# Optimization experiments

Measured on AMD Instinct MI355X. Metric: run time of the kernel, lower is better.

Reference implementation:

```python
import jax, jax.numpy as jnp
import numpy as np

N_KERNELS = 21
N_LAYERS = 2
N_HEADS = 8
ATT_DIM = 32
FF_HID = 100
EMB = 300


def kernel_mus(n):
    mus = [1.0]
    bin_size = 2.0 / (n - 1)
    mus.append(1.0 - bin_size / 2.0)
    for _ in range(1, n - 1):
        mus.append(mus[-1] - bin_size)
    return np.array(mus, dtype=np.float32)


def kernel_sigmas(n):
    return np.array([0.001] + [0.1] * (n - 1), dtype=np.float32)


def setup_inputs() -> dict:
    key = jax.random.key(0)
    ks = jax.random.split(key, 12)
    B, LQ, LD = 32, 64, 512
    u = lambda k, s, a: jax.random.uniform(k, s, jnp.float32, -a, a)
    return dict(
        q_embed=jax.random.normal(ks[0], (B, LQ, EMB), jnp.float32),
        d_embed=jax.random.normal(ks[1], (B, LD, EMB), jnp.float32),
        mask_q=(jax.random.uniform(ks[2], (B, LQ)) > 0.1).astype(jnp.float32),
        mask_d=(jax.random.uniform(ks[3], (B, LD)) > 0.1).astype(jnp.float32),
        mixer=jnp.full((1, 1, 1), 0.5, jnp.float32),
        nn_scaler=jnp.full((1,), 0.01, jnp.float32),
        ff_w1=u(ks[4], (N_LAYERS, EMB, FF_HID), 0.05),
        ff_b1=jnp.zeros((N_LAYERS, FF_HID), jnp.float32),
        ff_w2=u(ks[5], (N_LAYERS, FF_HID, EMB), 0.05),
        ff_b2=jnp.zeros((N_LAYERS, EMB), jnp.float32),
        ln1_g=jnp.ones((N_LAYERS, EMB), jnp.float32),
        ln1_b=jnp.zeros((N_LAYERS, EMB), jnp.float32),
        att_w=u(ks[6], (N_LAYERS, EMB, 3 * ATT_DIM), 0.05),
        att_b=jnp.zeros((N_LAYERS, 3 * ATT_DIM), jnp.float32),
        out_w=u(ks[7], (N_LAYERS, ATT_DIM, EMB), 0.05),
        out_b=jnp.zeros((N_LAYERS, EMB), jnp.float32),
        ln2_g=jnp.ones((N_LAYERS, EMB), jnp.float32),
        ln2_b=jnp.zeros((N_LAYERS, EMB), jnp.float32),
        dense_w=u(ks[8], (1, N_KERNELS), 0.014),
    )


def _layer_norm(x, g, b, eps=1e-6):
    m = jnp.mean(x, -1, keepdims=True)
    s = jnp.std(x, -1, keepdims=True, ddof=1)  # torch std is unbiased
    return g * (x - m) / (s + eps) + b


def _encoder(x, mask, p):
    # AllenNLP StackedSelfAttentionEncoder: [FF -> res+LN -> MHSA -> res+LN] x2
    B, T, E = x.shape
    scale = jnp.sqrt(jnp.float32(E // N_HEADS))
    hd = ATT_DIM // N_HEADS
    for l in range(N_LAYERS):
        h = jax.nn.relu(x @ p['ff_w1'][l] + p['ff_b1'][l]) @ p['ff_w2'][l] + p['ff_b2'][l]
        h = _layer_norm(h + x, p['ln1_g'][l], p['ln1_b'][l])
        c = h @ p['att_w'][l] + p['att_b'][l]              # [B,T,3*ATT_DIM]
        q = c[..., :ATT_DIM].reshape(B, T, N_HEADS, hd)
        k = c[..., ATT_DIM:2 * ATT_DIM].reshape(B, T, N_HEADS, hd)
        v = c[..., 2 * ATT_DIM:].reshape(B, T, N_HEADS, hd)
        sims = jnp.einsum('bqhd,bkhd->bhqk', q / scale, k)
        m = mask[:, None, None, :]
        att = jax.nn.softmax(sims * m, axis=-1) * m         # AllenNLP masked_softmax
        att = att / (jnp.sum(att, -1, keepdims=True) + 1e-13)
        o = jnp.einsum('bhqk,bkhd->bqhd', att, v).reshape(B, T, ATT_DIM)
        o = o @ p['out_w'][l] + p['out_b'][l]
        x = _layer_norm(o + h, p['ln2_g'][l], p['ln2_b'][l])
    return x


def reference(q_embed, d_embed, mask_q, mask_d, mixer, nn_scaler,
              ff_w1, ff_b1, ff_w2, ff_b2, ln1_g, ln1_b,
              att_w, att_b, out_w, out_b, ln2_g, ln2_b, dense_w):
    p = dict(ff_w1=ff_w1, ff_b1=ff_b1, ff_w2=ff_w2, ff_b2=ff_b2,
             ln1_g=ln1_g, ln1_b=ln1_b, att_w=att_w, att_b=att_b,
             out_w=out_w, out_b=out_b, ln2_g=ln2_g, ln2_b=ln2_b)
    mu = jnp.asarray(kernel_mus(N_KERNELS))        # [K]
    sigma = jnp.asarray(kernel_sigmas(N_KERNELS))  # [K]
    mq = mask_q[..., None]
    md = mask_d[..., None]
    q = q_embed * mq
    d = d_embed * md
    qc = _encoder(q, mask_q, p)
    dc = _encoder(d, mask_d, p)
    q = (mixer * q + (1.0 - mixer) * qc) * mq
    d = (mixer * d + (1.0 - mixer) * dc) * md
    qd_mask = mask_q[:, :, None] * mask_d[:, None, :]  # [B,Q,D]
    qn = q / (jnp.linalg.norm(q, axis=-1, keepdims=True) + 1e-13)
    dn = d / (jnp.linalg.norm(d, axis=-1, keepdims=True) + 1e-13)
    cos = jnp.einsum('bqe,bde->bqd', qn, dn) * qd_mask
    # Gaussian RBF soft histogram: [B,Q,D,K]
    kr = jnp.exp(-(cos[..., None] - mu) ** 2 / (2.0 * sigma ** 2)) * qd_mask[..., None]
    pkq = jnp.sum(kr, axis=2)                                 # [B,Q,K]
    log_pkq = jnp.log2(jnp.clip(pkq, 1e-10)) * nn_scaler
    per_kernel = jnp.sum(log_pkq * mq, axis=1)                # [B,K]
    return jnp.squeeze(per_kernel @ dense_w.T, axis=1)        # [B]
```

## Files before the change

### kernel.cpp

```cpp
#include <hip/hip_runtime.h>
#include <hip/hip_bf16.h>

#define BATCH 32
#define LQ 64
#define LD 512
#define EMB 300
#define FFH 100
#define ATTD 32
#define NH 8
#define NK 21
#define MQ (BATCH * LQ)
#define MD (BATCH * LD)
#define MALL (MQ + MD)

typedef __attribute__((ext_vector_type(8))) short bf16x8;
typedef __attribute__((ext_vector_type(4))) float f32x4;

__device__ __forceinline__ float wave_sum(float v) {
    #pragma unroll
    for (int off = 32; off > 0; off >>= 1) v += __shfl_xor(v, off);
    return v;
}

__device__ __forceinline__ float bf2f(__hip_bfloat16 h) {
    return __bfloat162float(h);
}

__device__ __forceinline__ float4 bf4_to_f4(const __hip_bfloat16* p) {
    uint2 u = *(const uint2*)p;
    float4 f;
    f.x = __uint_as_float((u.x & 0xffffu) << 16);
    f.y = __uint_as_float(u.x & 0xffff0000u);
    f.z = __uint_as_float((u.y & 0xffffu) << 16);
    f.w = __uint_as_float(u.y & 0xffff0000u);
    return f;
}

__global__ void maskmul_all(const float* __restrict__ q_embed, const float* __restrict__ d_embed,
                            const float* __restrict__ mask_q, const float* __restrict__ mask_d,
                            __hip_bfloat16* __restrict__ xbf, float* __restrict__ mall) {
    int i = blockIdx.x * blockDim.x + threadIdx.x;
    if (i >= MALL * EMB) return;
    int tok = i / EMB;
    float m, v;
    if (tok < MQ) {
        m = mask_q[tok];
        v = q_embed[i];
    } else {
        m = mask_d[tok - MQ];
        v = d_embed[i - MQ * EMB];
    }
    xbf[i] = __float2bfloat16(v * m);
    if (i % EMB == 0) mall[tok] = m;
}

__device__ __forceinline__ void conv_seg(const float* __restrict__ w, __hip_bfloat16* __restrict__ wt,
                                         int j, int K, int N) {
    int l = j / (K * N);
    int r = j % (K * N);
    int k = r / N, n = r % N;
    wt[(size_t)l * N * K + (size_t)n * K + k] = __float2bfloat16(w[j]);
}
__global__ void convert_all(const float* __restrict__ w1, const float* __restrict__ w2,
                            const float* __restrict__ aw, const float* __restrict__ ow,
                            __hip_bfloat16* __restrict__ w1t, __hip_bfloat16* __restrict__ w2t,
                            __hip_bfloat16* __restrict__ awt, __hip_bfloat16* __restrict__ owt) {
    int i = blockIdx.x * blockDim.x + threadIdx.x;
    const int S1 = 2 * EMB * FFH;
    const int S2 = S1 + 2 * FFH * EMB;
    const int S3 = S2 + 2 * EMB * 96;
    const int S4 = S3 + 2 * ATTD * EMB;
    if (i < S1)       conv_seg(w1, w1t, i, EMB, FFH);
    else if (i < S2)  conv_seg(w2, w2t, i - S1, FFH, EMB);
    else if (i < S3)  conv_seg(aw, awt, i - S2, EMB, 96);
    else if (i < S4)  conv_seg(ow, owt, i - S3, ATTD, EMB);
}

__device__ __forceinline__ void stage_row8(const __hip_bfloat16* __restrict__ src, bool rowvalid,
                                           int K, int gk, __hip_bfloat16* dst) {
    if (rowvalid && gk + 8 <= K) {
        const uint2* p = (const uint2*)(src + gk);
        uint2 a = p[0], b = p[1];
        *(uint2*)dst = a;
        *(uint2*)(dst + 4) = b;
    } else {
        #pragma unroll
        for (int j = 0; j < 8; j++)
            dst[j] = (rowvalid && gk + j < K) ? src[gk + j] : __float2bfloat16(0.f);
    }
}

template <bool RELU>
__global__ __launch_bounds__(256) void gemm_mfma(const __hip_bfloat16* __restrict__ A,
                                                 const __hip_bfloat16* __restrict__ Bt,
                                                 const float* __restrict__ bias,
                                                 __hip_bfloat16* __restrict__ Cb,
                                                 int M, int N, int K) {
    __shared__ __align__(16) __hip_bfloat16 As[64][40];
    __shared__ __align__(16) __hip_bfloat16 Bs[64][40];
    const int tid = threadIdx.x;
    const int m0 = blockIdx.y * 64, n0 = blockIdx.x * 64;
    const int lane = tid & 63;
    const int wv = tid >> 6;
    const int wm = wv >> 1, wn = wv & 1;
    const int l15 = lane & 15, lg = lane >> 4;
    const int srow = tid >> 2, sk8 = (tid & 3) * 8;
    f32x4 acc[2][2] = {};
    const int NS = (K + 31) >> 5;
    const __hip_bfloat16* arow = A + (size_t)(m0 + srow) * K;
    const bool bvalid = (n0 + srow) < N;
    const __hip_bfloat16* brow = Bt + (size_t)(n0 + srow) * K;

    for (int s = 0; s < NS; s++) {
        const int gk = (s << 5) + sk8;
        if (s) __syncthreads();
        stage_row8(arow, true, K, gk, &As[srow][sk8]);
        stage_row8(brow, bvalid, K, gk, &Bs[srow][sk8]);
        __syncthreads();
        bf16x8 af0 = *(const bf16x8*)&As[wm * 32 + l15][lg * 8];
        bf16x8 af1 = *(const bf16x8*)&As[wm * 32 + 16 + l15][lg * 8];
        bf16x8 bf0 = *(const bf16x8*)&Bs[wn * 32 + l15][lg * 8];
        bf16x8 bf1 = *(const bf16x8*)&Bs[wn * 32 + 16 + l15][lg * 8];
        acc[0][0] = __builtin_amdgcn_mfma_f32_16x16x32_bf16(af0, bf0, acc[0][0], 0, 0, 0);
        acc[0][1] = __builtin_amdgcn_mfma_f32_16x16x32_bf16(af0, bf1, acc[0][1], 0, 0, 0);
        acc[1][0] = __builtin_amdgcn_mfma_f32_16x16x32_bf16(af1, bf0, acc[1][0], 0, 0, 0);
        acc[1][1] = __builtin_amdgcn_mfma_f32_16x16x32_bf16(af1, bf1, acc[1][1], 0, 0, 0);
    }

    #pragma unroll
    for (int fc = 0; fc < 2; fc++) {
        int col = n0 + wn * 32 + fc * 16 + l15;
        if (col >= N) continue;
        float bs = bias[col];
        #pragma unroll
        for (int fr = 0; fr < 2; fr++) {
            int rbase = m0 + wm * 32 + fr * 16 + lg * 4;
            #pragma unroll
            for (int r = 0; r < 4; r++) {
                int row = rbase + r;
                float v = acc[fr][fc][r] + bs;
                if (RELU) v = fmaxf(v, 0.f);
                Cb[(size_t)row * N + col] = __float2bfloat16(v);
            }
        }
    }
}

__global__ __launch_bounds__(256) void gemm_ln(const __hip_bfloat16* __restrict__ A,
                                               const __hip_bfloat16* __restrict__ Bt,
                                               const float* __restrict__ bias,
                                               const __hip_bfloat16* __restrict__ Res,
                                               const float* __restrict__ g,
                                               const float* __restrict__ beta,
                                               __hip_bfloat16* __restrict__ Y,
                                               int M, int K) {
    __shared__ __align__(16) __hip_bfloat16 As[32][40];
    __shared__ __align__(16) __hip_bfloat16 Bs[320][40];
    __shared__ float red[2][4][32];
    const int tid = threadIdx.x;
    const int m0 = blockIdx.x * 32;
    const int lane = tid & 63;
    const int wv = tid >> 6;
    const int l15 = lane & 15, lg = lane >> 4;
    const int c0 = wv * 80;
    f32x4 acc[2][5] = {};
    const int NS = (K + 31) >> 5;

    for (int s = 0; s < NS; s++) {
        const int gk0 = s << 5;
        if (s) __syncthreads();
        for (int ch = tid; ch < 1408; ch += 256) {
            if (ch < 128) {
                int row = ch >> 2, k8 = (ch & 3) * 8;
                stage_row8(A + (size_t)(m0 + row) * K, true, K, gk0 + k8, &As[row][k8]);
            } else {
                int cc = ch - 128;
                int row = cc >> 2, k8 = (cc & 3) * 8;
                stage_row8(Bt + (size_t)row * K, row < EMB, K, gk0 + k8, &Bs[row][k8]);
            }
        }
        __syncthreads();
        bf16x8 af[2], bfr[5];
        af[0] = *(const bf16x8*)&As[l15][lg * 8];
        af[1] = *(const bf16x8*)&As[16 + l15][lg * 8];
        #pragma unroll
        for (int fc = 0; fc < 5; fc++)
            bfr[fc] = *(const bf16x8*)&Bs[c0 + fc * 16 + l15][lg * 8];
        #pragma unroll
        for (int fr = 0; fr < 2; fr++)
            #pragma unroll
            for (int fc = 0; fc < 5; fc++)
                acc[fr][fc] = __builtin_amdgcn_mfma_f32_16x16x32_bf16(af[fr], bfr[fc], acc[fr][fc], 0, 0, 0);
    }

    float rs[2][4];
    #pragma unroll
    for (int fr = 0; fr < 2; fr++)
        #pragma unroll
        for (int r = 0; r < 4; r++) rs[fr][r] = 0.f;
    #pragma unroll
    for (int fc = 0; fc < 5; fc++) {
        int col = c0 + fc * 16 + l15;
        bool valid = col < EMB;
        float bs = valid ? bias[col] : 0.f;
        #pragma unroll
        for (int fr = 0; fr < 2; fr++) {
            int rowb = m0 + fr * 16 + lg * 4;
            #pragma unroll
            for (int r = 0; r < 4; r++) {
                float v = 0.f;
                if (valid) v = acc[fr][fc][r] + bs + bf2f(Res[(size_t)(rowb + r) * EMB + col]);
                acc[fr][fc][r] = v;
                rs[fr][r] += v;
            }
        }
    }
    #pragma unroll
    for (int fr = 0; fr < 2; fr++)
        #pragma unroll
        for (int r = 0; r < 4; r++)
            #pragma unroll
            for (int off = 1; off < 16; off <<= 1)
                rs[fr][r] += __shfl_xor(rs[fr][r], off);
    if (l15 == 0) {
        #pragma unroll
        for (int fr = 0; fr < 2; fr++)
            #pragma unroll
            for (int r = 0; r < 4; r++)
                red[0][wv][fr * 16 + lg * 4 + r] = rs[fr][r];
    }
    __syncthreads();
    float mean[2][4];
    #pragma unroll
    for (int fr = 0; fr < 2; fr++)
        #pragma unroll
        for (int r = 0; r < 4; r++) {
            int ri = fr * 16 + lg * 4 + r;
            mean[fr][r] = (red[0][0][ri] + red[0][1][ri] + red[0][2][ri] + red[0][3][ri]) * (1.f / EMB);
        }
    float rq[2][4];
    #pragma unroll
    for (int fr = 0; fr < 2; fr++)
        #pragma unroll
        for (int r = 0; r < 4; r++) rq[fr][r] = 0.f;
    #pragma unroll
    for (int fc = 0; fc < 5; fc++) {
        int col = c0 + fc * 16 + l15;
        bool valid = col < EMB;
        #pragma unroll
        for (int fr = 0; fr < 2; fr++)
            #pragma unroll
            for (int r = 0; r < 4; r++) {
                if (valid) {
                    float d = acc[fr][fc][r] - mean[fr][r];
                    rq[fr][r] += d * d;
                }
            }
    }
    #pragma unroll
    for (int fr = 0; fr < 2; fr++)
        #pragma unroll
        for (int r = 0; r < 4; r++)
            #pragma unroll
            for (int off = 1; off < 16; off <<= 1)
                rq[fr][r] += __shfl_xor(rq[fr][r], off);
    if (l15 == 0) {
        #pragma unroll
        for (int fr = 0; fr < 2; fr++)
            #pragma unroll
            for (int r = 0; r < 4; r++)
                red[1][wv][fr * 16 + lg * 4 + r] = rq[fr][r];
    }
    __syncthreads();
    float inv[2][4];
    #pragma unroll
    for (int fr = 0; fr < 2; fr++)
        #pragma unroll
        for (int r = 0; r < 4; r++) {
            int ri = fr * 16 + lg * 4 + r;
            float tot = red[1][0][ri] + red[1][1][ri] + red[1][2][ri] + red[1][3][ri];
            float stdv = sqrtf(tot * (1.f / (EMB - 1)));
            inv[fr][r] = 1.f / (stdv + 1e-6f);
        }
    #pragma unroll
    for (int fc = 0; fc < 5; fc++) {
        int col = c0 + fc * 16 + l15;
        if (col >= EMB) continue;
        float gv = g[col], bv = beta[col];
        #pragma unroll
        for (int fr = 0; fr < 2; fr++) {
            int rowb = m0 + fr * 16 + lg * 4;
            #pragma unroll
            for (int r = 0; r < 4; r++) {
                float y = gv * (acc[fr][fc][r] - mean[fr][r]) * inv[fr][r] + bv;
                Y[(size_t)(rowb + r) * EMB + col] = __float2bfloat16(y);
            }
        }
    }
}

template <int T, int RPB, int KS>
__device__ __forceinline__ void attn_body(const __hip_bfloat16* __restrict__ cseg,
                                          const float* __restrict__ mask,
                                          __hip_bfloat16* __restrict__ oseg,
                                          int bh, int rb, char* smem) {
    constexpr int BLK = 512;
    float4* Ks = (float4*)smem;
    float4* Vs = Ks + T;
    float* part = (float*)(Vs + T);
    float* nmask_s = part + RPB * 5 * (KS - 1);
    const int b = bh / NH, h = bh % NH;
    const int tid = threadIdx.x;
    const __hip_bfloat16* base = cseg + (size_t)b * T * 96;

    if (tid == 0) *nmask_s = 0.f;
    __syncthreads();
    float lnm = 0.f;
    for (int j = tid; j < T; j += BLK) {
        float m = mask[b * T + j];
        float4 kv = bf4_to_f4(base + (size_t)j * 96 + ATTD + h * 4);
        float4 vv = bf4_to_f4(base + (size_t)j * 96 + 2 * ATTD + h * 4);
        kv.x *= m; kv.y *= m; kv.z *= m; kv.w *= m;
        vv.x *= m; vv.y *= m; vv.z *= m; vv.w *= m;
        Ks[j] = kv;
        Vs[j] = vv;
        lnm += 1.f - m;
    }
    lnm = wave_sum(lnm);
    if ((tid & 63) == 0 && lnm != 0.f) atomicAdd(nmask_s, lnm);
    __syncthreads();

    const int r = rb * RPB + (tid % RPB);
    const int ks = tid / RPB;
    const float inv_scale = 0.16439898730535729f;
    float4 qv = bf4_to_f4(base + (size_t)r * 96 + h * 4);
    qv.x *= inv_scale; qv.y *= inv_scale; qv.z *= inv_scale; qv.w *= inv_scale;

    float Sall = 0.f, ox = 0.f, oy = 0.f, oz = 0.f, ow = 0.f;
    constexpr int KC = T / KS;
    const int k0 = ks * KC;
    #pragma unroll 4
    for (int k = k0; k < k0 + KC; k++) {
        float4 kv = Ks[k];
        float4 vv = Vs[k];
        float s = fmaf(qv.x, kv.x, fmaf(qv.y, kv.y, fmaf(qv.z, kv.z, qv.w * kv.w)));
        float e = __expf(s);
        Sall += e;
        ox = fmaf(e, vv.x, ox);
        oy = fmaf(e, vv.y, oy);
        oz = fmaf(e, vv.z, oz);
        ow = fmaf(e, vv.w, ow);
    }
    if (ks > 0) {
        float* p = &part[((ks - 1) * RPB + (tid % RPB)) * 5];
        p[0] = Sall; p[1] = ox; p[2] = oy; p[3] = oz; p[4] = ow;
    }
    __syncthreads();
    if (ks == 0) {
        #pragma unroll
        for (int s2 = 0; s2 < KS - 1; s2++) {
            const float* p = &part[(s2 * RPB + r - rb * RPB) * 5];
            Sall += p[0]; ox += p[1]; oy += p[2]; oz += p[3]; ow += p[4];
        }
        float Sm = Sall - *nmask_s;
        float inv = 1.f / (Sm + 1e-13f * Sall);
        __hip_bfloat16* op = oseg + (size_t)(b * T + r) * ATTD + h * 4;
        op[0] = __float2bfloat16(ox * inv);
        op[1] = __float2bfloat16(oy * inv);
        op[2] = __float2bfloat16(oz * inv);
        op[3] = __float2bfloat16(ow * inv);
    }
}

__global__ __launch_bounds__(512) void attn_both(const __hip_bfloat16* __restrict__ cbf,
                                                 const float* __restrict__ mask_q,
                                                 const float* __restrict__ mask_d,
                                                 __hip_bfloat16* __restrict__ o32) {
    __shared__ __align__(16) char smem[24576];
    int blk = blockIdx.x;
    if (blk < BATCH * NH) {
        attn_body<LQ, 64, 8>(cbf, mask_q, o32, blk, 0, smem);
    } else {
        int bid = blk - BATCH * NH;
        attn_body<LD, 128, 4>(cbf + (size_t)MQ * 96, mask_d, o32 + (size_t)MQ * ATTD,
                              bid >> 2, bid & 3, smem);
    }
}

__global__ __launch_bounds__(256) void cos_mfma(const __hip_bfloat16* __restrict__ Qn,
                                                const __hip_bfloat16* __restrict__ Dn,
                                                float* __restrict__ Cos) {
    __shared__ __align__(16) __hip_bfloat16 As[64][40];
    __shared__ __align__(16) __hip_bfloat16 Bs[64][40];
    const int b = blockIdx.y;
    const int n0 = blockIdx.x * 64;
    const int tid = threadIdx.x;
    const int lane = tid & 63;
    const int wv = tid >> 6;
    const int wm = wv >> 1, wn = wv & 1;
    const int l15 = lane & 15, lg = lane >> 4;
    const int srow = tid >> 2, sk8 = (tid & 3) * 8;
    f32x4 acc[2][2] = {};
    const int NS = (EMB + 31) >> 5;
    const __hip_bfloat16* arow = Qn + ((size_t)b * LQ + srow) * EMB;
    const __hip_bfloat16* brow = Dn + ((size_t)b * LD + n0 + srow) * EMB;

    for (int s = 0; s < NS; s++) {
        const int gk = (s << 5) + sk8;
        if (s) __syncthreads();
        stage_row8(arow, true, EMB, gk, &As[srow][sk8]);
        stage_row8(brow, true, EMB, gk, &Bs[srow][sk8]);
        __syncthreads();
        bf16x8 af0 = *(const bf16x8*)&As[wm * 32 + l15][lg * 8];
        bf16x8 af1 = *(const bf16x8*)&As[wm * 32 + 16 + l15][lg * 8];
        bf16x8 bf0 = *(const bf16x8*)&Bs[wn * 32 + l15][lg * 8];
        bf16x8 bf1 = *(const bf16x8*)&Bs[wn * 32 + 16 + l15][lg * 8];
        acc[0][0] = __builtin_amdgcn_mfma_f32_16x16x32_bf16(af0, bf0, acc[0][0], 0, 0, 0);
        acc[0][1] = __builtin_amdgcn_mfma_f32_16x16x32_bf16(af0, bf1, acc[0][1], 0, 0, 0);
        acc[1][0] = __builtin_amdgcn_mfma_f32_16x16x32_bf16(af1, bf0, acc[1][0], 0, 0, 0);
        acc[1][1] = __builtin_amdgcn_mfma_f32_16x16x32_bf16(af1, bf1, acc[1][1], 0, 0, 0);
    }

    float* cb = Cos + (size_t)b * LQ * LD;
    #pragma unroll
    for (int fc = 0; fc < 2; fc++) {
        int col = n0 + wn * 32 + fc * 16 + l15;
        #pragma unroll
        for (int fr = 0; fr < 2; fr++) {
            int rbase = wm * 32 + fr * 16 + lg * 4;
            #pragma unroll
            for (int r = 0; r < 4; r++) {
                cb[(size_t)(rbase + r) * LD + col] = acc[fr][fc][r];
            }
        }
    }
}

__global__ __launch_bounds__(256) void mixnorm_bf(const __hip_bfloat16* __restrict__ x,
                                                  const __hip_bfloat16* __restrict__ xc,
                                                  const float* __restrict__ mask,
                                                  const float* __restrict__ mixer,
                                                  __hip_bfloat16* __restrict__ out) {
    int wid = (blockIdx.x * 256 + threadIdx.x) >> 6;
    int lane = threadIdx.x & 63;
    float mixv = mixer[0];
    float mval = mask[wid];
    const __hip_bfloat16* xr = x + (size_t)wid * EMB;
    const __hip_bfloat16* xcr = xc + (size_t)wid * EMB;
    float v[5];
    float s2 = 0.f;
    #pragma unroll
    for (int r = 0; r < 5; r++) {
        int idx = lane + r * 64;
        float val = 0.f;
        if (idx < EMB) val = (mixv * bf2f(xr[idx]) + (1.f - mixv) * bf2f(xcr[idx])) * mval;
        v[r] = val;
        s2 += val * val;
    }
    s2 = wave_sum(s2);
    float inv = 1.f / (sqrtf(s2) + 1e-13f);
    __hip_bfloat16* o = out + (size_t)wid * EMB;
    #pragma unroll
    for (int r = 0; r < 5; r++) {
        int idx = lane + r * 64;
        if (idx < EMB) o[idx] = __float2bfloat16(v[r] * inv);
    }
}

__global__ __launch_bounds__(256) void pool_kernel(const float* __restrict__ Cos,
                                                   const float* __restrict__ mask_q,
                                                   const float* __restrict__ mask_d,
                                                   const float* __restrict__ nn_scaler,
                                                   float* __restrict__ lp) {
    int wid = (blockIdx.x * 256 + threadIdx.x) >> 6;
    int lane = threadIdx.x & 63;
    int b = wid >> 6, qi = wid & 63;
    const float* crow = Cos + ((size_t)b * LQ + qi) * LD;
    const float* md = mask_d + b * LD;
    float acc[NK];
    #pragma unroll
    for (int k = 0; k < NK; k++) acc[k] = 0.f;
    #pragma unroll
    for (int rr = 0; rr < LD / 64; rr++) {
        int dj = rr * 64 + lane;
        float m = md[dj];
        if (m != 0.f) {
            float cv = crow[dj];
            float d0 = cv - 1.0f;
            acc[0] += __expf(d0 * d0 * -500000.0f);
            #pragma unroll
            for (int g = 0; g < 4; g++) {
                float mu_a = 0.95f - 0.5f * g;
                float dc = cv - mu_a;
                float t = __expf(dc * dc * -50.0f);
                float r = __expf(fmaf(-10.0f, dc, -0.5f));
                #pragma unroll
                for (int j = 0; j < 5; j++) {
                    acc[1 + 5 * g + j] += t;
                    t *= r;
                    r *= 0.36787944117144233f;
                }
            }
        }
    }
    float mq = mask_q[b * LQ + qi];
    float ns = nn_scaler[0];
    #pragma unroll
    for (int k = 0; k < NK; k++) {
        float s = wave_sum(acc[k]);
        if (lane == 0) lp[((size_t)b * LQ + qi) * NK + k] = log2f(fmaxf(s, 1e-10f)) * ns * mq;
    }
}

__global__ void final_kernel(const float* __restrict__ lp, const float* __restrict__ dense_w,
                             float* __restrict__ out) {
    int b = blockIdx.x;
    int t = threadIdx.x;
    float s = 0.f;
    if (t < NK) {
        for (int qi = 0; qi < LQ; qi++) s += lp[((size_t)b * LQ + qi) * NK + t];
        s *= dense_w[t];
    }
    s = wave_sum(s);
    if (t == 0) out[b] = s;
}

extern "C" void kernel_launch(void* const* d_in, const int* in_sizes, int n_in,
                              void* d_out, int out_size, void* d_ws, size_t ws_size,
                              hipStream_t stream) {
    (void)in_sizes; (void)n_in; (void)out_size; (void)ws_size;
    const float* q_embed  = (const float*)d_in[0];
    const float* d_embed  = (const float*)d_in[1];
    const float* mask_q   = (const float*)d_in[2];
    const float* mask_d   = (const float*)d_in[3];
    const float* mixer    = (const float*)d_in[4];
    const float* nn_scaler= (const float*)d_in[5];
    const float* ff_w1    = (const float*)d_in[6];
    const float* ff_b1    = (const float*)d_in[7];
    const float* ff_w2    = (const float*)d_in[8];
    const float* ff_b2    = (const float*)d_in[9];
    const float* ln1_g    = (const float*)d_in[10];
    const float* ln1_b    = (const float*)d_in[11];
    const float* att_w    = (const float*)d_in[12];
    const float* att_b    = (const float*)d_in[13];
    const float* out_w    = (const float*)d_in[14];
    const float* out_b    = (const float*)d_in[15];
    const float* ln2_g    = (const float*)d_in[16];
    const float* ln2_b    = (const float*)d_in[17];
    const float* dense_w  = (const float*)d_in[18];
    float* out = (float*)d_out;

    float* ws   = (float*)d_ws;
    float* cosb = ws;
    float* lp   = cosb + 1048576;
    float* mall = lp + 43008;
    __hip_bfloat16* xbf   = (__hip_bfloat16*)(mall + MALL);
    __hip_bfloat16* xcbf  = xbf  + (size_t)MALL * EMB;
    __hip_bfloat16* xc2bf = xcbf + (size_t)MALL * EMB;
    __hip_bfloat16* hbf   = xc2bf + (size_t)MALL * EMB;
    __hip_bfloat16* t1bf  = hbf  + (size_t)MALL * EMB;
    __hip_bfloat16* cbf   = t1bf + (size_t)MALL * FFH;
    __hip_bfloat16* o32bf = cbf  + (size_t)MALL * 96;
    __hip_bfloat16* w1t   = o32bf + (size_t)MALL * ATTD;
    __hip_bfloat16* w2t   = w1t + 2 * FFH * EMB;
    __hip_bfloat16* awt   = w2t + 2 * EMB * FFH;
    __hip_bfloat16* owt   = awt + 2 * 96 * EMB;

    convert_all<<<(196800 + 255) / 256, 256, 0, stream>>>(ff_w1, ff_w2, att_w, out_w,
                                                          w1t, w2t, awt, owt);
    maskmul_all<<<(MALL * EMB + 255) / 256, 256, 0, stream>>>(q_embed, d_embed, mask_q, mask_d,
                                                              xbf, mall);

    const __hip_bfloat16* xcur = xbf;
    for (int l = 0; l < 2; l++) {
        __hip_bfloat16* xout = (l == 0) ? xcbf : xc2bf;
        gemm_mfma<true><<<dim3(2, MALL / 64), 256, 0, stream>>>(
            xcur, w1t + (size_t)l * FFH * EMB, ff_b1 + l * FFH, t1bf, MALL, FFH, EMB);
        gemm_ln<<<MALL / 32, 256, 0, stream>>>(
            t1bf, w2t + (size_t)l * EMB * FFH, ff_b2 + l * EMB, xcur,
            ln1_g + l * EMB, ln1_b + l * EMB, hbf, MALL, FFH);
        gemm_mfma<false><<<dim3(2, MALL / 64), 256, 0, stream>>>(
            hbf, awt + (size_t)l * 96 * EMB, att_b + l * 96, cbf, MALL, 96, EMB);
        attn_both<<<BATCH * NH + BATCH * NH * (LD / 128), 512, 0, stream>>>(
            cbf, mask_q, mask_d, o32bf);
        gemm_ln<<<MALL / 32, 256, 0, stream>>>(
            o32bf, owt + (size_t)l * EMB * ATTD, out_b + l * EMB, hbf,
            ln2_g + l * EMB, ln2_b + l * EMB, xout, MALL, ATTD);
        xcur = xout;
    }

    mixnorm_bf<<<MALL / 4, 256, 0, stream>>>(xbf, xc2bf, mall, mixer, hbf);

    cos_mfma<<<dim3(LD / 64, BATCH), 256, 0, stream>>>(hbf, hbf + (size_t)MQ * EMB, cosb);

    pool_kernel<<<(BATCH * LQ) / 4, 256, 0, stream>>>(cosb, mask_q, mask_d, nn_scaler, lp);

    final_kernel<<<BATCH, 64, 0, stream>>>(lp, dense_w, out);
}
```

Before: 242.5 us.

## Replace LDS-staged GEMM+LayerNorm with direct-load per-wave full-row kernel

The GEMM+LayerNorm kernel now has each wave compute 16 full rows (19 MFMA column tiles) with operands loaded straight from global memory, so LDS staging, the cross-wave shared-memory reductions and their barriers are gone. Weight and intermediate buffers are zero-padded to 128 and 320 columns so the K dimension needs no bounds checks. The FF1 GEMM writes a padded 128-stride output for this purpose. The cost is higher register pressure (76 accumulator floats per lane) and redundant global/L2 reads of B across waves.

After: 243.0 us. Within noise of the previous version (+0.2%).

```diff
diff --git a/kernel.cpp b/kernel.cpp
--- a/kernel.cpp
+++ b/kernel.cpp
@@ -67,13 +67,28 @@
                             __hip_bfloat16* __restrict__ awt, __hip_bfloat16* __restrict__ owt) {
     int i = blockIdx.x * blockDim.x + threadIdx.x;
     const int S1 = 2 * EMB * FFH;
-    const int S2 = S1 + 2 * FFH * EMB;
+    const int S2 = S1 + 2 * 320 * 128;
     const int S3 = S2 + 2 * EMB * 96;
-    const int S4 = S3 + 2 * ATTD * EMB;
-    if (i < S1)       conv_seg(w1, w1t, i, EMB, FFH);
-    else if (i < S2)  conv_seg(w2, w2t, i - S1, FFH, EMB);
-    else if (i < S3)  conv_seg(aw, awt, i - S2, EMB, 96);
-    else if (i < S4)  conv_seg(ow, owt, i - S3, ATTD, EMB);
+    const int S4 = S3 + 2 * 320 * 32;
+    if (i < S1) {
+        conv_seg(w1, w1t, i, EMB, FFH);
+    } else if (i < S2) {
+        int j = i - S1;
+        int l = j / (320 * 128);
+        int r = j % (320 * 128);
+        int n = r / 128, k = r % 128;
+        float v = (n < EMB && k < FFH) ? w2[(size_t)l * FFH * EMB + (size_t)k * EMB + n] : 0.f;
+        w2t[j] = __float2bfloat16(v);
+    } else if (i < S3) {
+        conv_seg(aw, awt, i - S2, EMB, 96);
+    } else if (i < S4) {
+        int j = i - S3;
+        int l = j / (320 * 32);
+        int r = j % (320 * 32);
+        int n = r / 32, k = r % 32;
+        float v = (n < EMB && k < ATTD) ? ow[(size_t)l * ATTD * EMB + (size_t)k * EMB + n] : 0.f;
+        owt[j] = __float2bfloat16(v);
+    }
 }
 
 __device__ __forceinline__ void stage_row8(const __hip_bfloat16* __restrict__ src, bool rowvalid,
@@ -95,7 +110,7 @@
                                                  const __hip_bfloat16* __restrict__ Bt,
                                                  const float* __restrict__ bias,
                                                  __hip_bfloat16* __restrict__ Cb,
-                                                 int M, int N, int K) {
+                                                 int M, int Nr, int Ns, int K) {
     __shared__ __align__(16) __hip_bfloat16 As[64][40];
     __shared__ __align__(16) __hip_bfloat16 Bs[64][40];
     const int tid = threadIdx.x;
@@ -108,7 +123,7 @@
     f32x4 acc[2][2] = {};
     const int NS = (K + 31) >> 5;
     const __hip_bfloat16* arow = A + (size_t)(m0 + srow) * K;
-    const bool bvalid = (n0 + srow) < N;
+    const bool bvalid = (n0 + srow) < Nr;
     const __hip_bfloat16* brow = Bt + (size_t)(n0 + srow) * K;
 
     for (int s = 0; s < NS; s++) {
@@ -130,260 +145,103 @@
     #pragma unroll
     for (int fc = 0; fc < 2; fc++) {
         int col = n0 + wn * 32 + fc * 16 + l15;
-        if (col >= N) continue;
-        float bs = bias[col];
+        if (col >= Ns) continue;
+        float bs = (col < Nr) ? bias[col] : 0.f;
         #pragma unroll
         for (int fr = 0; fr < 2; fr++) {
             int rbase = m0 + wm * 32 + fr * 16 + lg * 4;
             #pragma unroll
             for (int r = 0; r < 4; r++) {
-                int row = rbase + r;
                 float v = acc[fr][fc][r] + bs;
                 if (RELU) v = fmaxf(v, 0.f);
-                Cb[(size_t)row * N + col] = __float2bfloat16(v);
+                Cb[(size_t)(rbase + r) * Ns + col] = __float2bfloat16(v);
             }
         }
     }
 }
 
-__global__ __launch_bounds__(256) void gemm_ln(const __hip_bfloat16* __restrict__ A,
-                                               const __hip_bfloat16* __restrict__ Bt,
-                                               const float* __restrict__ bias,
-                                               const __hip_bfloat16* __restrict__ Res,
-                                               const float* __restrict__ g,
-                                               const float* __restrict__ beta,
-                                               __hip_bfloat16* __restrict__ Y,
-                                               int M, int K) {
-    __shared__ __align__(16) __hip_bfloat16 As[32][40];
-    __shared__ __align__(16) __hip_bfloat16 Bs[320][40];
-    __shared__ float red[2][4][32];
+template <int NSTEP, int KSTR, int ASTR>
+__global__ __launch_bounds__(256) void gemm_ln_direct(const __hip_bfloat16* __restrict__ A,
+                                                      const __hip_bfloat16* __restrict__ Bt,
+                                                      const float* __restrict__ bias,
+                                                      const __hip_bfloat16* __restrict__ Res,
+                                                      const float* __restrict__ g,
+                                                      const float* __restrict__ beta,
+                                                      __hip_bfloat16* __restrict__ Y) {
     const int tid = threadIdx.x;
-    const int m0 = blockIdx.x * 32;
+    const int wv = tid >> 6;
     const int lane = tid & 63;
-    const int wv = tid >> 6;
     const int l15 = lane & 15, lg = lane >> 4;
-    const int c0 = wv * 80;
-    f32x4 acc[2][5] = {};
-    const int NS = (K + 31) >> 5;
-
-    for (int s = 0; s < NS; s++) {
-        const int gk0 = s << 5;
-        if (s) __syncthreads();
-        for (int ch = tid; ch < 1408; ch += 256) {
-            if (ch < 128) {
-                int row = ch >> 2, k8 = (ch & 3) * 8;
-                stage_row8(A + (size_t)(m0 + row) * K, true, K, gk0 + k8, &As[row][k8]);
-            } else {
-                int cc = ch - 128;
-                int row = cc >> 2, k8 = (cc & 3) * 8;
-                stage_row8(Bt + (size_t)row * K, row < EMB, K, gk0 + k8, &Bs[row][k8]);
-            }
-        }
-        __syncthreads();
-        bf16x8 af[2], bfr[5];
-        af[0] = *(const bf16x8*)&As[l15][lg * 8];
-        af[1] = *(const bf16x8*)&As[16 + l15][lg * 8];
-        #pragma unroll
-        for (int fc = 0; fc < 5; fc++)
-            bfr[fc] = *(const bf16x8*)&Bs[c0 + fc * 16 + l15][lg * 8];
-        #pragma unroll
-        for (int fr = 0; fr < 2; fr++)
-            #pragma unroll
-            for (int fc = 0; fc < 5; fc++)
-                acc[fr][fc] = __builtin_amdgcn_mfma_f32_16x16x32_bf16(af[fr], bfr[fc], acc[fr][fc], 0, 0, 0);
-    }
-
-    float rs[2][4];
-    #pragma unroll
-    for (int fr = 0; fr < 2; fr++)
-        #pragma unroll
-        for (int r = 0; r < 4; r++) rs[fr][r] = 0.f;
-    #pragma unroll
-    for (int fc = 0; fc < 5; fc++) {
-        int col = c0 + fc * 16 + l15;
+    const int m0 = blockIdx.x * 64 + wv * 16;
+
+    f32x4 acc[19];
+    #pragma unroll
+    for (int fc = 0; fc < 19; fc++) acc[fc] = (f32x4){0.f, 0.f, 0.f, 0.f};
+
+    #pragma unroll
+    for (int ks = 0; ks < NSTEP; ks++) {
+        const int kb = ks * 32 + lg * 8;
+        bf16x8 af = *(const bf16x8*)(A + (size_t)(m0 + l15) * ASTR + kb);
+        #pragma unroll
+        for (int fc = 0; fc < 19; fc++) {
+            bf16x8 bf = *(const bf16x8*)(Bt + (size_t)(fc * 16 + l15) * KSTR + kb);
+            acc[fc] = __builtin_amdgcn_mfma_f32_16x16x32_bf16(af, bf, acc[fc], 0, 0, 0);
+        }
+    }
+
+    float rs[4] = {0.f, 0.f, 0.f, 0.f};
+    #pragma unroll
+    for (int fc = 0; fc < 19; fc++) {
+        int col = fc * 16 + l15;
         bool valid = col < EMB;
         float bs = valid ? bias[col] : 0.f;
         #pragma unroll
-        for (int fr = 0; fr < 2; fr++) {
-            int rowb = m0 + fr * 16 + lg * 4;
+        for (int r = 0; r < 4; r++) {
+            float v = 0.f;
+            if (valid) v = acc[fc][r] + bs + bf2f(Res[(size_t)(m0 + lg * 4 + r) * EMB + col]);
+            acc[fc][r] = v;
+            rs[r] += v;
+        }
+    }
+    #pragma unroll
+    for (int r = 0; r < 4; r++)
+        #pragma unroll
+        for (int off = 1; off < 16; off <<= 1)
+            rs[r] += __shfl_xor(rs[r], off);
+    float mean[4], invv[4];
+    #pragma unroll
+    for (int r = 0; r < 4; r++) mean[r] = rs[r] * (1.f / EMB);
+
+    float rq[4] = {0.f, 0.f, 0.f, 0.f};
+    #pragma unroll
+    for (int fc = 0; fc < 19; fc++) {
+        int col = fc * 16 + l15;
+        if (col < EMB) {
             #pragma unroll
             for (int r = 0; r < 4; r++) {
-                float v = 0.f;
-                if (valid) v = acc[fr][fc][r] + bs + bf2f(Res[(size_t)(rowb + r) * EMB + col]);
-                acc[fr][fc][r] = v;
-                rs[fr][r] += v;
+                float d = acc[fc][r] - mean[r];
+                rq[r] += d * d;
             }
         }
     }
     #pragma unroll
-    for (int fr = 0; fr < 2; fr++)
-        #pragma unroll
-        for (int r = 0; r < 4; r++)
-            #pragma unroll
-            for (int off = 1; off < 16; off <<= 1)
-                rs[fr][r] += __shfl_xor(rs[fr][r], off);
-    if (l15 == 0) {
-        #pragma unroll
-        for (int fr = 0; fr < 2; fr++)
-            #pragma unroll
-            for (int r = 0; r < 4; r++)
-                red[0][wv][fr * 16 + lg * 4 + r] = rs[fr][r];
-    }
-    __syncthreads();
-    float mean[2][4];
-    #pragma unroll
-    for (int fr = 0; fr < 2; fr++)
-        #pragma unroll
-        for (int r = 0; r < 4; r++) {
-            int ri = fr * 16 + lg * 4 + r;
-            mean[fr][r] = (red[0][0][ri] + red[0][1][ri] + red[0][2][ri] + red[0][3][ri]) * (1.f / EMB);
-        }
-    float rq[2][4];
-    #pragma unroll
-    for (int fr = 0; fr < 2; fr++)
-        #pragma unroll
-        for (int r = 0; r < 4; r++) rq[fr][r] = 0.f;
-    #pragma unroll
-    for (int fc = 0; fc < 5; fc++) {
-        int col = c0 + fc * 16 + l15;
-        bool valid = col < EMB;
-        #pragma unroll
-        for (int fr = 0; fr < 2; fr++)
-            #pragma unroll
-            for (int r = 0; r < 4; r++) {
-                if (valid) {
-                    float d = acc[fr][fc][r] - mean[fr][r];
-                    rq[fr][r] += d * d;
-                }
-            }
-    }
-    #pragma unroll
-    for (int fr = 0; fr < 2; fr++)
-        #pragma unroll
-        for (int r = 0; r < 4; r++)
-            #pragma unroll
-            for (int off = 1; off < 16; off <<= 1)
-                rq[fr][r] += __shfl_xor(rq[fr][r], off);
-    if (l15 == 0) {
-        #pragma unroll
-        for (int fr = 0; fr < 2; fr++)
-            #pragma unroll
-            for (int r = 0; r < 4; r++)
-                red[1][wv][fr * 16 + lg * 4 + r] = rq[fr][r];
-    }
-    __syncthreads();
-    float inv[2][4];
-    #pragma unroll
-    for (int fr = 0; fr < 2; fr++)
-        #pragma unroll
-        for (int r = 0; r < 4; r++) {
-            int ri = fr * 16 + lg * 4 + r;
-            float tot = red[1][0][ri] + red[1][1][ri] + red[1][2][ri] + red[1][3][ri];
-            float stdv = sqrtf(tot * (1.f / (EMB - 1)));
-            inv[fr][r] = 1.f / (stdv + 1e-6f);
-        }
-    #pragma unroll
-    for (int fc = 0; fc < 5; fc++) {
-        int col = c0 + fc * 16 + l15;
+    for (int r = 0; r < 4; r++) {
+        #pragma unroll
+        for (int off = 1; off < 16; off <<= 1)
+            rq[r] += __shfl_xor(rq[r], off);
+        float stdv = sqrtf(rq[r] * (1.f / (EMB - 1)));
+        invv[r] = 1.f / (stdv + 1e-6f);
+    }
+    #pragma unroll
+    for (int fc = 0; fc < 19; fc++) {
+        int col = fc * 16 + l15;
         if (col >= EMB) continue;
         float gv = g[col], bv = beta[col];
         #pragma unroll
-        for (int fr = 0; fr < 2; fr++) {
-            int rowb = m0 + fr * 16 + lg * 4;
-            #pragma unroll
-            for (int r = 0; r < 4; r++) {
-                float y = gv * (acc[fr][fc][r] - mean[fr][r]) * inv[fr][r] + bv;
-                Y[(size_t)(rowb + r) * EMB + col] = __float2bfloat16(y);
-            }
-        }
-    }
-}
-
-template <int T, int RPB, int KS>
-__device__ __forceinline__ void attn_body(const __hip_bfloat16* __restrict__ cseg,
-                                          const float* __restrict__ mask,
-                                          __hip_bfloat16* __restrict__ oseg,
-                                          int bh, int rb, char* smem) {
-    constexpr int BLK = 512;
-    float4* Ks = (float4*)smem;
-    float4* Vs = Ks + T;
-    float* part = (float*)(Vs + T);
-    float* nmask_s = part + RPB * 5 * (KS - 1);
-    const int b = bh / NH, h = bh % NH;
-    const int tid = threadIdx.x;
-    const __hip_bfloat16* base = cseg + (size_t)b * T * 96;
-
-    if (tid == 0) *nmask_s = 0.f;
-    __syncthreads();
-    float lnm = 0.f;
-    for (int j = tid; j < T; j += BLK) {
-        float m = mask[b * T + j];
-        float4 kv = bf4_to_f4(base + (size_t)j * 96 + ATTD + h * 4);
-        float4 vv = bf4_to_f4(base + (size_t)j * 96 + 2 * ATTD + h * 4);
-        kv.x *= m; kv.y *= m; kv.z *= m; kv.w *= m;
-        vv.x *= m; vv.y *= m; vv.z *= m; vv.w *= m;
-        Ks[j] = kv;
-        Vs[j] = vv;
-        lnm += 1.f - m;
-    }
-    lnm = wave_sum(lnm);
-    if ((tid & 63) == 0 && lnm != 0.f) atomicAdd(nmask_s, lnm);
-    __syncthreads();
-
-    const int r = rb * RPB + (tid % RPB);
-    const int ks = tid / RPB;
-    const float inv_scale = 0.16439898730535729f;
-    float4 qv = bf4_to_f4(base + (size_t)r * 96 + h * 4);
-    qv.x *= inv_scale; qv.y *= inv_scale; qv.z *= inv_scale; qv.w *= inv_scale;
-
-    float Sall = 0.f, ox = 0.f, oy = 0.f, oz = 0.f, ow = 0.f;
-    constexpr int KC = T / KS;
-    const int k0 = ks * KC;
-    #pragma unroll 4
-    for (int k = k0; k < k0 + KC; k++) {
-        float4 kv = Ks[k];
-        float4 vv = Vs[k];
-        float s = fmaf(qv.x, kv.x, fmaf(qv.y, kv.y, fmaf(qv.z, kv.z, qv.w * kv.w)));
-        float e = __expf(s);
-        Sall += e;
-        ox = fmaf(e, vv.x, ox);
-        oy = fmaf(e, vv.y, oy);
-        oz = fmaf(e, vv.z, oz);
-        ow = fmaf(e, vv.w, ow);
-    }
-    if (ks > 0) {
-        float* p = &part[((ks - 1) * RPB + (tid % RPB)) * 5];
-        p[0] = Sall; p[1] = ox; p[2] = oy; p[3] = oz; p[4] = ow;
-    }
-    __syncthreads();
-    if (ks == 0) {
-        #pragma unroll
-        for (int s2 = 0; s2 < KS - 1; s2++) {
-            const float* p = &part[(s2 * RPB + r - rb * RPB) * 5];
-            Sall += p[0]; ox += p[1]; oy += p[2]; oz += p[3]; ow += p[4];
-        }
-        float Sm = Sall - *nmask_s;
-        float inv = 1.f / (Sm + 1e-13f * Sall);
-        __hip_bfloat16* op = oseg + (size_t)(b * T + r) * ATTD + h * 4;
-        op[0] = __float2bfloat16(ox * inv);
-        op[1] = __float2bfloat16(oy * inv);
-        op[2] = __float2bfloat16(oz * inv);
-        op[3] = __float2bfloat16(ow * inv);
-    }
-}
-
-__global__ __launch_bounds__(512) void attn_both(const __hip_bfloat16* __restrict__ cbf,
-                                                 const float* __restrict__ mask_q,
-                                                 const float* __restrict__ mask_d,
-                                                 __hip_bfloat16* __restrict__ o32) {
-    __shared__ __align__(16) char smem[24576];
-    int blk = blockIdx.x;
-    if (blk < BATCH * NH) {
-        attn_body<LQ, 64, 8>(cbf, mask_q, o32, blk, 0, smem);
-    } else {
-        int bid = blk - BATCH * NH;
-        attn_body<LD, 128, 4>(cbf + (size_t)MQ * 96, mask_d, o32 + (size_t)MQ * ATTD,
-                              bid >> 2, bid & 3, smem);
+        for (int r = 0; r < 4; r++) {
+            float y = gv * (acc[fc][r] - mean[r]) * invv[r] + bv;
+            Y[(size_t)(m0 + lg * 4 + r) * EMB + col] = __float2bfloat16(y);
+        }
     }
 }
 
@@ -433,6 +291,94 @@
                 cb[(size_t)(rbase + r) * LD + col] = acc[fr][fc][r];
             }
         }
+    }
+}
+
+template <int T, int RPB, int KS>
+__device__ __forceinline__ void attn_body(const __hip_bfloat16* __restrict__ cseg,
+                                          const float* __restrict__ mask,
+                                          __hip_bfloat16* __restrict__ oseg,
+                                          int bh, int rb, char* smem) {
+    constexpr int BLK = 512;
+    float4* Ks = (float4*)smem;
+    float4* Vs = Ks + T;
+    float* part = (float*)(Vs + T);
+    float* nmask_s = part + RPB * 5 * (KS - 1);
+    const int b = bh / NH, h = bh % NH;
+    const int tid = threadIdx.x;
+    const __hip_bfloat16* base = cseg + (size_t)b * T * 96;
+
+    if (tid == 0) *nmask_s = 0.f;
+    __syncthreads();
+    float lnm = 0.f;
+    for (int j = tid; j < T; j += BLK) {
+        float m = mask[b * T + j];
+        float4 kv = bf4_to_f4(base + (size_t)j * 96 + ATTD + h * 4);
+        float4 vv = bf4_to_f4(base + (size_t)j * 96 + 2 * ATTD + h * 4);
+        kv.x *= m; kv.y *= m; kv.z *= m; kv.w *= m;
+        vv.x *= m; vv.y *= m; vv.z *= m; vv.w *= m;
+        Ks[j] = kv;
+        Vs[j] = vv;
+        lnm += 1.f - m;
+    }
+    lnm = wave_sum(lnm);
+    if ((tid & 63) == 0 && lnm != 0.f) atomicAdd(nmask_s, lnm);
+    __syncthreads();
+
+    const int r = rb * RPB + (tid % RPB);
+    const int ks = tid / RPB;
+    const float inv_scale = 0.16439898730535729f;
+    float4 qv = bf4_to_f4(base + (size_t)r * 96 + h * 4);
+    qv.x *= inv_scale; qv.y *= inv_scale; qv.z *= inv_scale; qv.w *= inv_scale;
+
+    float Sall = 0.f, ox = 0.f, oy = 0.f, oz = 0.f, ow = 0.f;
+    constexpr int KC = T / KS;
+    const int k0 = ks * KC;
+    #pragma unroll 4
+    for (int k = k0; k < k0 + KC; k++) {
+        float4 kv = Ks[k];
+        float4 vv = Vs[k];
+        float s = fmaf(qv.x, kv.x, fmaf(qv.y, kv.y, fmaf(qv.z, kv.z, qv.w * kv.w)));
+        float e = __expf(s);
+        Sall += e;
+        ox = fmaf(e, vv.x, ox);
+        oy = fmaf(e, vv.y, oy);
+        oz = fmaf(e, vv.z, oz);
+        ow = fmaf(e, vv.w, ow);
+    }
+    if (ks > 0) {
+        float* p = &part[((ks - 1) * RPB + (tid % RPB)) * 5];
+        p[0] = Sall; p[1] = ox; p[2] = oy; p[3] = oz; p[4] = ow;
+    }
+    __syncthreads();
+    if (ks == 0) {
+        #pragma unroll
+        for (int s2 = 0; s2 < KS - 1; s2++) {
+            const float* p = &part[(s2 * RPB + r - rb * RPB) * 5];
+            Sall += p[0]; ox += p[1]; oy += p[2]; oz += p[3]; ow += p[4];
+        }
+        float Sm = Sall - *nmask_s;
+        float inv = 1.f / (Sm + 1e-13f * Sall);
+        __hip_bfloat16* op = oseg + (size_t)(b * T + r) * ATTD + h * 4;
+        op[0] = __float2bfloat16(ox * inv);
+        op[1] = __float2bfloat16(oy * inv);
+        op[2] = __float2bfloat16(oz * inv);
+        op[3] = __float2bfloat16(ow * inv);
+    }
+}
+
+__global__ __launch_bounds__(512) void attn_both(const __hip_bfloat16* __restrict__ cbf,
+                                                 const float* __restrict__ mask_q,
+                                                 const float* __restrict__ mask_d,
+                                                 __hip_bfloat16* __restrict__ o32) {
+    __shared__ __align__(16) char smem[24576];
+    int blk = blockIdx.x;
+    if (blk < BATCH * NH) {
+        attn_body<LQ, 64, 8>(cbf, mask_q, o32, blk, 0, smem);
+    } else {
+        int bid = blk - BATCH * NH;
+        attn_body<LD, 128, 4>(cbf + (size_t)MQ * 96, mask_d, o32 + (size_t)MQ * ATTD,
+                              bid >> 2, bid & 3, smem);
     }
 }
 
@@ -559,14 +505,14 @@
     __hip_bfloat16* xc2bf = xcbf + (size_t)MALL * EMB;
     __hip_bfloat16* hbf   = xc2bf + (size_t)MALL * EMB;
     __hip_bfloat16* t1bf  = hbf  + (size_t)MALL * EMB;
-    __hip_bfloat16* cbf   = t1bf + (size_t)MALL * FFH;
+    __hip_bfloat16* cbf   = t1bf + (size_t)MALL * 128;
     __hip_bfloat16* o32bf = cbf  + (size_t)MALL * 96;
     __hip_bfloat16* w1t   = o32bf + (size_t)MALL * ATTD;
     __hip_bfloat16* w2t   = w1t + 2 * FFH * EMB;
-    __hip_bfloat16* awt   = w2t + 2 * EMB * FFH;
+    __hip_bfloat16* awt   = w2t + 2 * 320 * 128;
     __hip_bfloat16* owt   = awt + 2 * 96 * EMB;
 
-    convert_all<<<(196800 + 255) / 256, 256, 0, stream>>>(ff_w1, ff_w2, att_w, out_w,
+    convert_all<<<(220000 + 255) / 256, 256, 0, stream>>>(ff_w1, ff_w2, att_w, out_w,
                                                           w1t, w2t, awt, owt);
     maskmul_all<<<(MALL * EMB + 255) / 256, 256, 0, stream>>>(q_embed, d_embed, mask_q, mask_d,
                                                               xbf, mall);
@@ -575,17 +521,17 @@
     for (int l = 0; l < 2; l++) {
         __hip_bfloat16* xout = (l == 0) ? xcbf : xc2bf;
         gemm_mfma<true><<<dim3(2, MALL / 64), 256, 0, stream>>>(
-            xcur, w1t + (size_t)l * FFH * EMB, ff_b1 + l * FFH, t1bf, MALL, FFH, EMB);
-        gemm_ln<<<MALL / 32, 256, 0, stream>>>(
-            t1bf, w2t + (size_t)l * EMB * FFH, ff_b2 + l * EMB, xcur,
-            ln1_g + l * EMB, ln1_b + l * EMB, hbf, MALL, FFH);
+            xcur, w1t + (size_t)l * FFH * EMB, ff_b1 + l * FFH, t1bf, MALL, FFH, 128, EMB);
+        gemm_ln_direct<4, 128, 128><<<MALL / 64, 256, 0, stream>>>(
+            t1bf, w2t + (size_t)l * 320 * 128, ff_b2 + l * EMB, xcur,
+            ln1_g + l * EMB, ln1_b + l * EMB, hbf);
         gemm_mfma<false><<<dim3(2, MALL / 64), 256, 0, stream>>>(
-            hbf, awt + (size_t)l * 96 * EMB, att_b + l * 96, cbf, MALL, 96, EMB);
+            hbf, awt + (size_t)l * 96 * EMB, att_b + l * 96, cbf, MALL, 96, 96, EMB);
         attn_both<<<BATCH * NH + BATCH * NH * (LD / 128), 512, 0, stream>>>(
             cbf, mask_q, mask_d, o32bf);
-        gemm_ln<<<MALL / 32, 256, 0, stream>>>(
-            o32bf, owt + (size_t)l * EMB * ATTD, out_b + l * EMB, hbf,
-            ln2_g + l * EMB, ln2_b + l * EMB, xout, MALL, ATTD);
+        gemm_ln_direct<1, 32, 32><<<MALL / 64, 256, 0, stream>>>(
+            o32bf, owt + (size_t)l * 320 * 32, out_b + l * EMB, hbf,
+            ln2_g + l * EMB, ln2_b + l * EMB, xout);
         xcur = xout;
     }
 
```
